# Kernel tuning notes

Hardware: AMD Instinct MI355X
Metric: run time of the kernel (lower is better)

The kernel has to match this reference:

```python
import jax, jax.numpy as jnp
import numpy as np

NUM_HEADS = 16
CHUNK = 512


def setup_inputs() -> dict:
    key = jax.random.key(0)
    k1, k2, k3 = jax.random.split(key, 3)
    B, S, H = 2, 2048, 1024
    x = jax.random.normal(k1, (B, S, H), dtype=jnp.float32)
    w_qkv = jax.random.normal(k2, (H, 3 * H), dtype=jnp.float32) * 0.02
    b_qkv = jnp.zeros((3 * H,), dtype=jnp.float32)
    w_proj = jax.random.normal(k3, (H, H), dtype=jnp.float32) * 0.02
    b_proj = jnp.zeros((H,), dtype=jnp.float32)
    return {"x": x, "w_qkv": w_qkv, "b_qkv": b_qkv, "w_proj": w_proj, "b_proj": b_proj}


def reference(x, w_qkv, b_qkv, w_proj, b_proj):
    B, S, H = x.shape
    nh, cs = NUM_HEADS, CHUNK
    hd = H // nh
    nc = S // cs  # number of chunks (seq_len > chunk_size -> chunked branch)

    qkv = x @ w_qkv + b_qkv  # [B,S,3H]
    qkv = qkv.reshape(B, S, 3, nh, hd).transpose(2, 0, 3, 1, 4)  # [3,B,nh,S,hd]
    q, k, v = qkv[0], qkv[1], qkv[2]  # each [B,nh,S,hd]

    # split sequence into chunks: [B,nh,nc,cs,hd]
    qc = q.reshape(B, nh, nc, cs, hd)
    kc = k.reshape(B, nh, nc, cs, hd)
    vc = v.reshape(B, nh, nc, cs, hd)

    scale = 1.0 / jnp.sqrt(jnp.asarray(hd, dtype=x.dtype))
    # scores for every (q-chunk i, k-chunk j) pair: [B,nh,i,j,cs,cs]
    scores = jnp.einsum('bhicd,bhjed->bhijce', qc, kc) * scale
    # softmax is LOCAL to each k-chunk (per pair), matching the torch code
    attn = jax.nn.softmax(scores, axis=-1)
    # attend within each pair, then AVERAGE over k-chunks j
    out = jnp.einsum('bhijce,bhjed->bhicd', attn, vc) / nc  # [B,nh,nc,cs,hd]

    out = out.reshape(B, nh, S, hd).transpose(0, 2, 1, 3).reshape(B, S, H)
    # dropout is identity in eval mode
    return out @ w_proj + b_proj
```

## Files before the change

### kernel.cpp

```cpp
#include <hip/hip_runtime.h>
#include <hip/hip_bf16.h>
#include <stdint.h>

typedef __bf16 bf16;
typedef __bf16 bf16x8 __attribute__((ext_vector_type(8)));
typedef __bf16 bf16x4 __attribute__((ext_vector_type(4)));
typedef float f32x4 __attribute__((ext_vector_type(4)));

#define MFMA16(a, b, c) __builtin_amdgcn_mfma_f32_16x16x32_bf16(a, b, c, 0, 0, 0)
#define SBAR() __builtin_amdgcn_sched_barrier(0)

__device__ __forceinline__ void gload_lds16(const void* g, void* l) {
  __builtin_amdgcn_global_load_lds(
      (const __attribute__((address_space(1))) void*)g,
      (__attribute__((address_space(3))) void*)l, 16, 0, 0);
}


__global__ void f32_to_bf16_kernel(const float* __restrict__ in,
                                   bf16* __restrict__ out, int n) {
  int i = (blockIdx.x * blockDim.x + threadIdx.x) * 4;
  if (i >= n) return;
  const float4 v = *(const float4*)(in + i);
  bf16x4 o = {(bf16)v.x, (bf16)v.y, (bf16)v.z, (bf16)v.w};
  *(bf16x4*)(out + i) = o;
}

__global__ void transpose_to_bf16(const float* __restrict__ in,
                                  bf16* __restrict__ out, int R, int C) {
  __shared__ float t[32][33];
  const int tx = threadIdx.x, ty = threadIdx.y;
  const int c0 = blockIdx.x * 32, r0 = blockIdx.y * 32;
  for (int i = 0; i < 32; i += 8)
    t[ty + i][tx] = in[(size_t)(r0 + ty + i) * C + c0 + tx];
  __syncthreads();
  for (int i = 0; i < 32; i += 8)
    out[(size_t)(c0 + ty + i) * R + r0 + tx] = (bf16)t[tx][ty + i];
}

__global__ void reduce_ctx(const bf16* __restrict__ p1, bf16* __restrict__ ctx) {
  const int i = (blockIdx.x * blockDim.x + threadIdx.x) * 8;
  const bf16x8 a = *(const bf16x8*)(ctx + i);
  const bf16x8 b = *(const bf16x8*)(p1 + i);
  bf16x8 o;
#pragma unroll
  for (int j = 0; j < 8; ++j)
    o[j] = (bf16)(0.25f * ((float)a[j] + (float)b[j]));
  *(bf16x8*)(ctx + i) = o;
}


__global__ __launch_bounds__(512, 1) void gemm_qkv(
    const bf16* __restrict__ A, const bf16* __restrict__ Bt,
    const float* __restrict__ bias, bf16* __restrict__ qp,
    bf16* __restrict__ kp, bf16* __restrict__ vT) {
  __shared__ __align__(16) char lds[98304];
  const int tid = threadIdx.x;
  const int wid = tid >> 6, lane = tid & 63;
  const int l15 = lane & 15, g = lane >> 4;
  const int wr = wid >> 2, wc = wid & 3;
  const int wg = (blockIdx.x & 7) * 24 + (blockIdx.x >> 3);
  const int m0 = (wg / 12) * 256, n0 = (wg % 12) * 256;
  const int K = 1024, nt = 32;

  const int srow = tid >> 2;
  const int scol = (((tid & 3) ^ ((srow >> 1) & 3)) * 8);

  auto ldsA = [&](int bi) { return lds + bi * 32768; };
  auto ldsB = [&](int bi) { return lds + bi * 32768 + 16384; };

  auto stageA = [&](int t) {
    const int bi = t % 3, kt = t * 32;
    const bf16* s0 = A + (size_t)(m0 + srow) * K + kt + scol;
    gload_lds16(s0, ldsA(bi) + (size_t)tid * 16);
    gload_lds16(s0 + (size_t)128 * K, ldsA(bi) + 8192 + (size_t)tid * 16);
  };
  auto stageB = [&](int t) {
    const int bi = t % 3, kt = t * 32;
    const bf16* s0 = Bt + (size_t)(n0 + srow) * K + kt + scol;
    gload_lds16(s0, ldsB(bi) + (size_t)tid * 16);
    gload_lds16(s0 + (size_t)128 * K, ldsB(bi) + 8192 + (size_t)tid * 16);
  };

  f32x4 acc[8][4] = {};

  stageA(0);
  stageB(0);
  stageA(1);
  stageB(1);

  const int swzr = ((l15 >> 1) & 3) << 4;

#pragma unroll 1
  for (int t = 0; t < nt; ++t) {
    const int bi = t % 3;
    if (t < nt - 1)
      asm volatile("s_waitcnt vmcnt(4)" ::: "memory");
    else
      asm volatile("s_waitcnt vmcnt(0)" ::: "memory");
    __builtin_amdgcn_s_barrier();
    bf16x8 Bf[4], Af[4];
#pragma unroll
    for (int ni = 0; ni < 4; ++ni)
      Bf[ni] = *(const bf16x8*)(ldsB(bi) + (wc * 64 + ni * 16 + l15) * 64 +
                                ((g * 16) ^ swzr));
#pragma unroll
    for (int mi = 0; mi < 4; ++mi)
      Af[mi] = *(const bf16x8*)(ldsA(bi) + (wr * 128 + mi * 16 + l15) * 64 +
                                ((g * 16) ^ swzr));
    if (t + 2 < nt) stageA(t + 2);
    __builtin_amdgcn_s_setprio(1);
#pragma unroll
    for (int mi = 0; mi < 4; ++mi)
#pragma unroll
      for (int ni = 0; ni < 4; ++ni)
        acc[mi][ni] = MFMA16(Af[mi], Bf[ni], acc[mi][ni]);
    __builtin_amdgcn_s_setprio(0);
#pragma unroll
    for (int mi = 0; mi < 4; ++mi)
      Af[mi] = *(const bf16x8*)(ldsA(bi) +
                                (wr * 128 + 64 + mi * 16 + l15) * 64 +
                                ((g * 16) ^ swzr));
    if (t + 2 < nt) stageB(t + 2);
    __builtin_amdgcn_s_setprio(1);
#pragma unroll
    for (int mi = 0; mi < 4; ++mi)
#pragma unroll
      for (int ni = 0; ni < 4; ++ni)
        acc[4 + mi][ni] = MFMA16(Af[mi], Bf[ni], acc[4 + mi][ni]);
    __builtin_amdgcn_s_setprio(0);
  }

  const int b = m0 >> 11;
  if (n0 >= 2048) {
    __builtin_amdgcn_s_barrier();
    bf16* T = (bf16*)lds + (size_t)wid * (64 * 68);
    const int hh = (n0 - 2048 + wc * 64) >> 6;
#pragma unroll
    for (int half = 0; half < 2; ++half) {
      const int sbase = (m0 & 2047) + wr * 128 + half * 64;
#pragma unroll
      for (int ni = 0; ni < 4; ++ni) {
        const float bv = bias[n0 + wc * 64 + ni * 16 + l15];
#pragma unroll
        for (int mi = 0; mi < 4; ++mi)
#pragma unroll
          for (int rg = 0; rg < 4; ++rg)
            T[(ni * 16 + l15) * 68 + mi * 16 + g * 4 + rg] =
                (bf16)(acc[half * 4 + mi][ni][rg] + bv);
      }
      __builtin_amdgcn_s_barrier();
      bf16* vrow = vT + ((size_t)(b * 16 + hh) * 64) * 2048 + sbase;
#pragma unroll
      for (int rr = 0; rr < 16; ++rr) {
        const int d = rr * 4 + g;
        const bf16x4 v4 = *(const bf16x4*)(T + d * 68 + l15 * 4);
        *(bf16x4*)(vrow + (size_t)d * 2048 + l15 * 4) = v4;
      }
      __builtin_amdgcn_s_barrier();
    }
  } else {
    const int sec = n0 >> 10;
    bf16* dst = (sec == 0) ? qp : kp;
    const float qscale = (sec == 0) ? 0.1803368801f : 1.0f;
#pragma unroll
    for (int mi = 0; mi < 8; ++mi) {
      const int rbase = m0 + wr * 128 + mi * 16 + g * 4;
#pragma unroll
      for (int ni = 0; ni < 4; ++ni) {
        const int cc = n0 + wc * 64 + ni * 16 + l15;
        const float bv = bias[cc];
        const int hh = (cc >> 6) & 15, d = cc & 63;
#pragma unroll
        for (int rg = 0; rg < 4; ++rg) {
          const int r = rbase + rg;
          const int s = r & 2047;
          dst[((size_t)(b * 16 + hh) * 2048 + s) * 64 + d] =
              (bf16)((acc[mi][ni][rg] + bv) * qscale);
        }
      }
    }
  }
}


__global__ __launch_bounds__(256, 2) void gemm_proj(
    const bf16* __restrict__ A, const bf16* __restrict__ Bt,
    const float* __restrict__ bias, float* __restrict__ Cout, int M, int N,
    int K, int nxb) {
  __shared__ __align__(16) char smem[65536];
  const int tid = threadIdx.x;
  const int wid = tid >> 6, lane = tid & 63;
  const int l15 = lane & 15, g = lane >> 4;
  const int cpx = gridDim.x >> 3;
  const int wg = (blockIdx.x & 7) * cpx + (blockIdx.x >> 3);
  const int m0 = (wg / nxb) * 128, n0 = (wg % nxb) * 128;
  const int wr = wid >> 1, wc = wid & 1;
  const int nt = K / 64;

  const int soff = wid * 4096 + lane * 16;

  auto stage = [&](int t, int buf) {
    const int kt = t * 64;
    char* bufA = smem + buf * 32768;
    char* bufB = bufA + 16384;
#pragma unroll
    for (int c = 0; c < 4; ++c) {
      const int off = soff + c * 1024;
      const int e = off >> 1;
      const int r = e >> 6, col = e & 63;
      gload_lds16(A + (size_t)(m0 + r) * K + kt + col, bufA + off);
      gload_lds16(Bt + (size_t)(n0 + r) * K + kt + col, bufB + off);
    }
  };

  f32x4 acc[4][4] = {};

  stage(0, 0);

#pragma unroll 1
  for (int t = 0; t < nt; ++t) {
    __syncthreads();
    SBAR();
    if (t + 1 < nt) stage(t + 1, (t + 1) & 1);
    const bf16* lA = (const bf16*)(smem + (t & 1) * 32768);
    const bf16* lB = (const bf16*)(smem + (t & 1) * 32768 + 16384);
#pragma unroll
    for (int kk = 0; kk < 2; ++kk) {
      const int ko = kk * 32 + g * 8;
      bf16x8 af[4], bfr[4];
#pragma unroll
      for (int mi = 0; mi < 4; ++mi)
        af[mi] = *(const bf16x8*)(lA + (wr * 64 + mi * 16 + l15) * 64 + ko);
#pragma unroll
      for (int ni = 0; ni < 4; ++ni)
        bfr[ni] = *(const bf16x8*)(lB + (wc * 64 + ni * 16 + l15) * 64 + ko);
      __builtin_amdgcn_s_setprio(1);
#pragma unroll
      for (int mi = 0; mi < 4; ++mi)
#pragma unroll
        for (int ni = 0; ni < 4; ++ni)
          acc[mi][ni] = MFMA16(af[mi], bfr[ni], acc[mi][ni]);
      __builtin_amdgcn_s_setprio(0);
    }
  }

#pragma unroll
  for (int mi = 0; mi < 4; ++mi) {
    const int rbase = m0 + wr * 64 + mi * 16 + g * 4;
#pragma unroll
    for (int ni = 0; ni < 4; ++ni) {
      const int cc = n0 + wc * 64 + ni * 16 + l15;
      const float bv = bias[cc];
#pragma unroll
      for (int rg = 0; rg < 4; ++rg)
        Cout[(size_t)(rbase + rg) * N + cc] = acc[mi][ni][rg] + bv;
    }
  }
}


__global__ __launch_bounds__(256, 4) void attn_kernel(
    const bf16* __restrict__ qp, const bf16* __restrict__ kp,
    const bf16* __restrict__ vT, bf16* __restrict__ p0,
    bf16* __restrict__ p1) {
  __shared__ __align__(16) char lds_raw[32768];

  const int tid = threadIdx.x;
  const int wid = tid >> 6, lane = tid & 63;
  const int l15 = lane & 15, g = lane >> 4;
  const int wg = (blockIdx.x & 7) * 128 + (blockIdx.x >> 3);
  const int ch = wg & 1, qt = (wg >> 1) & 15, bhh = wg >> 5;
  const int h = bhh & 15, b = bhh >> 4;
  const size_t bh = (size_t)bhh;
  const int rowbase = b * 2048 + qt * 128;

  const bf16* qptr = qp + (bh * 2048 + (size_t)qt * 128 + wid * 32) * 64;
  bf16x8 Qf[2][2];
#pragma unroll
  for (int m = 0; m < 2; ++m)
#pragma unroll
    for (int hf = 0; hf < 2; ++hf)
      Qf[m][hf] =
          *(const bf16x8*)(qptr + (size_t)(m * 16 + l15) * 64 + hf * 32 + g * 8);

  bf16x8 ones;
#pragma unroll
  for (int i = 0; i < 8; ++i) ones[i] = (bf16)1.0f;

  const bf16* kbase = kp + bh * 2048 * 64;
  const bf16* vbase = vT + bh * 64 * 2048;

  const int srow = lane >> 3;
  const int scol = 8 * ((lane & 7) ^ srow);
  char* ldsK = lds_raw;
  char* ldsV = lds_raw + 16384;

  auto stage = [&](int tile, int buf) {
    const int r0 = wid * 16 + srow;
    const bf16* ks = kbase + ((size_t)tile * 64 + r0) * 64 + scol;
    char* kd = ldsK + buf * 8192 + wid * 2048;
    gload_lds16(ks, kd);
    gload_lds16(ks + 8 * 64, kd + 1024);
    const bf16* vs = vbase + (size_t)r0 * 2048 + tile * 64 + scol;
    char* vd = ldsV + buf * 8192 + wid * 2048;
    gload_lds16(vs, vd);
    gload_lds16(vs + 8 * 2048, vd + 1024);
  };

  f32x4 Otot[2][4] = {};
  const int swz = (l15 & 7) << 4;

  stage(ch * 16, 0);

#pragma unroll 1
  for (int c2 = 0; c2 < 2; ++c2) {
    f32x4 Och[2][4] = {};
    f32x4 ssum[2] = {};
#pragma unroll 1
    for (int h8 = 0; h8 < 8; ++h8) {
      const int t = c2 * 8 + h8;
      __syncthreads();
      SBAR();
      stage(ch * 16 + ((t + 1) & 15), (t + 1) & 1);
      const char* Kt = ldsK + (t & 1) * 8192;
      const char* Vt = ldsV + (t & 1) * 8192;
#pragma unroll
      for (int kk2 = 0; kk2 < 2; ++kk2) {
        f32x4 sacc[2][2] = {};
        __builtin_amdgcn_s_setprio(1);
#pragma unroll
        for (int b2 = 0; b2 < 2; ++b2)
#pragma unroll
          for (int hf = 0; hf < 2; ++hf) {
            const bf16x8 kf =
                *(const bf16x8*)(Kt + ((kk2 * 2 + b2) * 16 + l15) * 128 +
                                 ((hf * 64 + g * 16) ^ swz));
            sacc[b2][0] = MFMA16(kf, Qf[0][hf], sacc[b2][0]);
            sacc[b2][1] = MFMA16(kf, Qf[1][hf], sacc[b2][1]);
          }
        __builtin_amdgcn_s_setprio(0);
        bf16x8 af[2];
#pragma unroll
        for (int m = 0; m < 2; ++m)
#pragma unroll
          for (int j = 0; j < 4; ++j) {
            af[m][j] = (bf16)__builtin_amdgcn_exp2f(sacc[0][m][j]);
            af[m][4 + j] = (bf16)__builtin_amdgcn_exp2f(sacc[1][m][j]);
          }
        __builtin_amdgcn_s_setprio(1);
#pragma unroll
        for (int n = 0; n < 4; ++n) {
          const char* vr = Vt + (n * 16 + l15) * 128;
          const bf16x4 lo = *(const bf16x4*)(vr + ((kk2 * 64 + g * 8) ^ swz));
          const bf16x4 hi =
              *(const bf16x4*)(vr + ((kk2 * 64 + 32 + g * 8) ^ swz));
          const bf16x8 vf =
              __builtin_shufflevector(lo, hi, 0, 1, 2, 3, 4, 5, 6, 7);
          Och[0][n] = MFMA16(af[0], vf, Och[0][n]);
          Och[1][n] = MFMA16(af[1], vf, Och[1][n]);
        }
        ssum[0] = MFMA16(af[0], ones, ssum[0]);
        ssum[1] = MFMA16(af[1], ones, ssum[1]);
        __builtin_amdgcn_s_setprio(0);
      }
    }
#pragma unroll
    for (int m = 0; m < 2; ++m)
#pragma unroll
      for (int rg = 0; rg < 4; ++rg) {
        const float inv = __builtin_amdgcn_rcpf(ssum[m][rg]);
#pragma unroll
        for (int n = 0; n < 4; ++n) Otot[m][n][rg] += Och[m][n][rg] * inv;
      }
  }

  bf16* pc = ch ? p1 : p0;
#pragma unroll
  for (int m = 0; m < 2; ++m)
#pragma unroll
    for (int n = 0; n < 4; ++n)
#pragma unroll
      for (int rg = 0; rg < 4; ++rg) {
        const int r = rowbase + wid * 32 + m * 16 + g * 4 + rg;
        pc[(size_t)r * 1024 + h * 64 + n * 16 + l15] = (bf16)Otot[m][n][rg];
      }
}


extern "C" void kernel_launch(void* const* d_in, const int* in_sizes, int n_in,
                              void* d_out, int out_size, void* d_ws,
                              size_t ws_size, hipStream_t stream) {
  const float* x = (const float*)d_in[0];
  const float* w_qkv = (const float*)d_in[1];
  const float* b_qkv = (const float*)d_in[2];
  const float* w_proj = (const float*)d_in[3];
  const float* b_proj = (const float*)d_in[4];
  float* out = (float*)d_out;

  char* ws = (char*)d_ws;
  bf16* xb     = (bf16*)(ws);
  bf16* wqkvT  = (bf16*)(ws + (8u << 20));
  bf16* wprojT = (bf16*)(ws + (14u << 20));
  bf16* qp     = (bf16*)(ws + (16u << 20));
  bf16* kp     = (bf16*)(ws + (24u << 20));
  bf16* vT     = (bf16*)(ws + (32u << 20));
  bf16* ctx    = (bf16*)(ws + (40u << 20));

  hipLaunchKernelGGL(f32_to_bf16_kernel, dim3(4096), dim3(256), 0, stream, x,
                     xb, 4096 * 1024);
  hipLaunchKernelGGL(transpose_to_bf16, dim3(96, 32), dim3(32, 8), 0, stream,
                     w_qkv, wqkvT, 1024, 3072);
  hipLaunchKernelGGL(transpose_to_bf16, dim3(32, 32), dim3(32, 8), 0, stream,
                     w_proj, wprojT, 1024, 1024);
  hipLaunchKernelGGL(gemm_qkv, dim3(192), dim3(512), 0, stream, xb, wqkvT,
                     b_qkv, qp, kp, vT);
  hipLaunchKernelGGL(attn_kernel, dim3(1024), dim3(256), 0, stream, qp, kp, vT,
                     ctx, xb);
  hipLaunchKernelGGL(reduce_ctx, dim3(2048), dim3(256), 0, stream, xb, ctx);
  hipLaunchKernelGGL(gemm_proj, dim3(8 * 32), dim3(256), 0, stream, ctx,
                     wprojT, b_proj, out, 4096, 1024, 1024, 8);
}
```

Measured before the change: 110.8 us.

## Fuse prep conversions into one launch and retile QKV GEMM to 128x128

Merges the x conversion and both weight transposes into a single prep kernel, removing two kernel launches. Rewrites the QKV GEMM from 256x256 tiles with 512 threads and a triple-buffered K=32 pipeline into 128x128 tiles with 256 threads, double-buffered K=64 stages, and two blocks per CU. This gives 768 blocks instead of 192, improving load balance across the CUs at the cost of lower per-block data reuse. The LDS XOR swizzle is dropped, which may introduce bank conflicts, and the software pipeline is now shallower.

```diff
diff --git a/kernel.cpp b/kernel.cpp
--- a/kernel.cpp
+++ b/kernel.cpp
@@ -17,25 +17,38 @@
 }
 
 
-__global__ void f32_to_bf16_kernel(const float* __restrict__ in,
-                                   bf16* __restrict__ out, int n) {
-  int i = (blockIdx.x * blockDim.x + threadIdx.x) * 4;
-  if (i >= n) return;
-  const float4 v = *(const float4*)(in + i);
-  bf16x4 o = {(bf16)v.x, (bf16)v.y, (bf16)v.z, (bf16)v.w};
-  *(bf16x4*)(out + i) = o;
-}
-
-__global__ void transpose_to_bf16(const float* __restrict__ in,
-                                  bf16* __restrict__ out, int R, int C) {
+__global__ void prep_kernel(const float* __restrict__ x, bf16* __restrict__ xb,
+                            const float* __restrict__ w_qkv,
+                            bf16* __restrict__ wqkvT,
+                            const float* __restrict__ w_proj,
+                            bf16* __restrict__ wprojT) {
   __shared__ float t[32][33];
-  const int tx = threadIdx.x, ty = threadIdx.y;
-  const int c0 = blockIdx.x * 32, r0 = blockIdx.y * 32;
-  for (int i = 0; i < 32; i += 8)
-    t[ty + i][tx] = in[(size_t)(r0 + ty + i) * C + c0 + tx];
-  __syncthreads();
-  for (int i = 0; i < 32; i += 8)
-    out[(size_t)(c0 + ty + i) * R + r0 + tx] = (bf16)t[tx][ty + i];
+  const int bid = blockIdx.x;
+  if (bid < 4096) {
+    const int i = (bid * 256 + threadIdx.x) * 4;
+    const float4 v = *(const float4*)(x + i);
+    bf16x4 o = {(bf16)v.x, (bf16)v.y, (bf16)v.z, (bf16)v.w};
+    *(bf16x4*)(xb + i) = o;
+  } else {
+    const float* in;
+    bf16* out;
+    int C, tile;
+    if (bid < 7168) {
+      in = w_qkv; out = wqkvT; C = 3072; tile = bid - 4096;
+    } else {
+      in = w_proj; out = wprojT; C = 1024; tile = bid - 7168;
+    }
+    const int ntx = C >> 5;
+    const int c0 = (tile % ntx) * 32, r0 = (tile / ntx) * 32;
+    const int tx = threadIdx.x & 31, ty = threadIdx.x >> 5;
+#pragma unroll
+    for (int i = 0; i < 32; i += 8)
+      t[ty + i][tx] = in[(size_t)(r0 + ty + i) * C + c0 + tx];
+    __syncthreads();
+#pragma unroll
+    for (int i = 0; i < 32; i += 8)
+      out[(size_t)(c0 + ty + i) * 1024 + r0 + tx] = (bf16)t[tx][ty + i];
+  }
 }
 
 __global__ void reduce_ctx(const bf16* __restrict__ p1, bf16* __restrict__ ctx) {
@@ -50,122 +63,96 @@
 }
 
 
-__global__ __launch_bounds__(512, 1) void gemm_qkv(
+__global__ __launch_bounds__(256, 2) void gemm_qkv(
     const bf16* __restrict__ A, const bf16* __restrict__ Bt,
     const float* __restrict__ bias, bf16* __restrict__ qp,
     bf16* __restrict__ kp, bf16* __restrict__ vT) {
-  __shared__ __align__(16) char lds[98304];
+  __shared__ __align__(16) char smem[65536];
   const int tid = threadIdx.x;
   const int wid = tid >> 6, lane = tid & 63;
   const int l15 = lane & 15, g = lane >> 4;
-  const int wr = wid >> 2, wc = wid & 3;
-  const int wg = (blockIdx.x & 7) * 24 + (blockIdx.x >> 3);
-  const int m0 = (wg / 12) * 256, n0 = (wg % 12) * 256;
-  const int K = 1024, nt = 32;
-
-  const int srow = tid >> 2;
-  const int scol = (((tid & 3) ^ ((srow >> 1) & 3)) * 8);
-
-  auto ldsA = [&](int bi) { return lds + bi * 32768; };
-  auto ldsB = [&](int bi) { return lds + bi * 32768 + 16384; };
-
-  auto stageA = [&](int t) {
-    const int bi = t % 3, kt = t * 32;
-    const bf16* s0 = A + (size_t)(m0 + srow) * K + kt + scol;
-    gload_lds16(s0, ldsA(bi) + (size_t)tid * 16);
-    gload_lds16(s0 + (size_t)128 * K, ldsA(bi) + 8192 + (size_t)tid * 16);
+  const int wg = (blockIdx.x & 7) * 96 + (blockIdx.x >> 3);
+  const int m0 = (wg / 24) * 128, n0 = (wg % 24) * 128;
+  const int wr = wid >> 1, wc = wid & 1;
+  const int K = 1024, nt = 16;
+
+  const int soff = wid * 4096 + lane * 16;
+
+  auto stage = [&](int t, int buf) {
+    const int kt = t * 64;
+    char* bufA = smem + buf * 32768;
+    char* bufB = bufA + 16384;
+#pragma unroll
+    for (int c = 0; c < 4; ++c) {
+      const int off = soff + c * 1024;
+      const int e = off >> 1;
+      const int r = e >> 6, col = e & 63;
+      gload_lds16(A + (size_t)(m0 + r) * K + kt + col, bufA + off);
+      gload_lds16(Bt + (size_t)(n0 + r) * K + kt + col, bufB + off);
+    }
   };
-  auto stageB = [&](int t) {
-    const int bi = t % 3, kt = t * 32;
-    const bf16* s0 = Bt + (size_t)(n0 + srow) * K + kt + scol;
-    gload_lds16(s0, ldsB(bi) + (size_t)tid * 16);
-    gload_lds16(s0 + (size_t)128 * K, ldsB(bi) + 8192 + (size_t)tid * 16);
-  };
-
-  f32x4 acc[8][4] = {};
-
-  stageA(0);
-  stageB(0);
-  stageA(1);
-  stageB(1);
-
-  const int swzr = ((l15 >> 1) & 3) << 4;
+
+  f32x4 acc[4][4] = {};
+
+  stage(0, 0);
 
 #pragma unroll 1
   for (int t = 0; t < nt; ++t) {
-    const int bi = t % 3;
-    if (t < nt - 1)
-      asm volatile("s_waitcnt vmcnt(4)" ::: "memory");
-    else
-      asm volatile("s_waitcnt vmcnt(0)" ::: "memory");
-    __builtin_amdgcn_s_barrier();
-    bf16x8 Bf[4], Af[4];
-#pragma unroll
-    for (int ni = 0; ni < 4; ++ni)
-      Bf[ni] = *(const bf16x8*)(ldsB(bi) + (wc * 64 + ni * 16 + l15) * 64 +
-                                ((g * 16) ^ swzr));
-#pragma unroll
-    for (int mi = 0; mi < 4; ++mi)
-      Af[mi] = *(const bf16x8*)(ldsA(bi) + (wr * 128 + mi * 16 + l15) * 64 +
-                                ((g * 16) ^ swzr));
-    if (t + 2 < nt) stageA(t + 2);
-    __builtin_amdgcn_s_setprio(1);
-#pragma unroll
-    for (int mi = 0; mi < 4; ++mi)
+    __syncthreads();
+    SBAR();
+    if (t + 1 < nt) stage(t + 1, (t + 1) & 1);
+    const bf16* lA = (const bf16*)(smem + (t & 1) * 32768);
+    const bf16* lB = (const bf16*)(smem + (t & 1) * 32768 + 16384);
+#pragma unroll
+    for (int kk = 0; kk < 2; ++kk) {
+      const int ko = kk * 32 + g * 8;
+      bf16x8 af[4], bfr[4];
+#pragma unroll
+      for (int mi = 0; mi < 4; ++mi)
+        af[mi] = *(const bf16x8*)(lA + (wr * 64 + mi * 16 + l15) * 64 + ko);
 #pragma unroll
       for (int ni = 0; ni < 4; ++ni)
-        acc[mi][ni] = MFMA16(Af[mi], Bf[ni], acc[mi][ni]);
-    __builtin_amdgcn_s_setprio(0);
-#pragma unroll
-    for (int mi = 0; mi < 4; ++mi)
-      Af[mi] = *(const bf16x8*)(ldsA(bi) +
-                                (wr * 128 + 64 + mi * 16 + l15) * 64 +
-                                ((g * 16) ^ swzr));
-    if (t + 2 < nt) stageB(t + 2);
-    __builtin_amdgcn_s_setprio(1);
-#pragma unroll
-    for (int mi = 0; mi < 4; ++mi)
-#pragma unroll
-      for (int ni = 0; ni < 4; ++ni)
-        acc[4 + mi][ni] = MFMA16(Af[mi], Bf[ni], acc[4 + mi][ni]);
-    __builtin_amdgcn_s_setprio(0);
-  }
-
+        bfr[ni] = *(const bf16x8*)(lB + (wc * 64 + ni * 16 + l15) * 64 + ko);
+      __builtin_amdgcn_s_setprio(1);
+#pragma unroll
+      for (int mi = 0; mi < 4; ++mi)
+#pragma unroll
+        for (int ni = 0; ni < 4; ++ni)
+          acc[mi][ni] = MFMA16(af[mi], bfr[ni], acc[mi][ni]);
+      __builtin_amdgcn_s_setprio(0);
+    }
+  }
+
+  __syncthreads();
   const int b = m0 >> 11;
   if (n0 >= 2048) {
-    __builtin_amdgcn_s_barrier();
-    bf16* T = (bf16*)lds + (size_t)wid * (64 * 68);
+    bf16* T = (bf16*)smem + (size_t)wid * (64 * 68);
+#pragma unroll
+    for (int ni = 0; ni < 4; ++ni) {
+      const float bv = bias[n0 + wc * 64 + ni * 16 + l15];
+#pragma unroll
+      for (int mi = 0; mi < 4; ++mi)
+#pragma unroll
+        for (int rg = 0; rg < 4; ++rg)
+          T[(ni * 16 + l15) * 68 + mi * 16 + g * 4 + rg] =
+              (bf16)(acc[mi][ni][rg] + bv);
+    }
     const int hh = (n0 - 2048 + wc * 64) >> 6;
-#pragma unroll
-    for (int half = 0; half < 2; ++half) {
-      const int sbase = (m0 & 2047) + wr * 128 + half * 64;
-#pragma unroll
-      for (int ni = 0; ni < 4; ++ni) {
-        const float bv = bias[n0 + wc * 64 + ni * 16 + l15];
-#pragma unroll
-        for (int mi = 0; mi < 4; ++mi)
-#pragma unroll
-          for (int rg = 0; rg < 4; ++rg)
-            T[(ni * 16 + l15) * 68 + mi * 16 + g * 4 + rg] =
-                (bf16)(acc[half * 4 + mi][ni][rg] + bv);
-      }
-      __builtin_amdgcn_s_barrier();
-      bf16* vrow = vT + ((size_t)(b * 16 + hh) * 64) * 2048 + sbase;
-#pragma unroll
-      for (int rr = 0; rr < 16; ++rr) {
-        const int d = rr * 4 + g;
-        const bf16x4 v4 = *(const bf16x4*)(T + d * 68 + l15 * 4);
-        *(bf16x4*)(vrow + (size_t)d * 2048 + l15 * 4) = v4;
-      }
-      __builtin_amdgcn_s_barrier();
+    const int sbase = (m0 & 2047) + wr * 64;
+    bf16* vrow = vT + ((size_t)(b * 16 + hh) * 64) * 2048 + sbase;
+#pragma unroll
+    for (int rr = 0; rr < 16; ++rr) {
+      const int d = rr * 4 + g;
+      const bf16x4 v4 = *(const bf16x4*)(T + d * 68 + l15 * 4);
+      *(bf16x4*)(vrow + (size_t)d * 2048 + l15 * 4) = v4;
     }
   } else {
     const int sec = n0 >> 10;
     bf16* dst = (sec == 0) ? qp : kp;
     const float qscale = (sec == 0) ? 0.1803368801f : 1.0f;
 #pragma unroll
-    for (int mi = 0; mi < 8; ++mi) {
-      const int rbase = m0 + wr * 128 + mi * 16 + g * 4;
+    for (int mi = 0; mi < 4; ++mi) {
+      const int rbase = m0 + wr * 64 + mi * 16 + g * 4;
 #pragma unroll
       for (int ni = 0; ni < 4; ++ni) {
         const int cc = n0 + wc * 64 + ni * 16 + l15;
@@ -407,13 +394,9 @@
   bf16* vT     = (bf16*)(ws + (32u << 20));
   bf16* ctx    = (bf16*)(ws + (40u << 20));
 
-  hipLaunchKernelGGL(f32_to_bf16_kernel, dim3(4096), dim3(256), 0, stream, x,
-                     xb, 4096 * 1024);
-  hipLaunchKernelGGL(transpose_to_bf16, dim3(96, 32), dim3(32, 8), 0, stream,
-                     w_qkv, wqkvT, 1024, 3072);
-  hipLaunchKernelGGL(transpose_to_bf16, dim3(32, 32), dim3(32, 8), 0, stream,
-                     w_proj, wprojT, 1024, 1024);
-  hipLaunchKernelGGL(gemm_qkv, dim3(192), dim3(512), 0, stream, xb, wqkvT,
+  hipLaunchKernelGGL(prep_kernel, dim3(8192), dim3(256), 0, stream, x, xb,
+                     w_qkv, wqkvT, w_proj, wprojT);
+  hipLaunchKernelGGL(gemm_qkv, dim3(768), dim3(256), 0, stream, xb, wqkvT,
                      b_qkv, qp, kp, vT);
   hipLaunchKernelGGL(attn_kernel, dim3(1024), dim3(256), 0, stream, qp, kp, vT,
                      ctx, xb);
```

New measurement: 111.1 us. About the same (+0.3%).
